# Performance work log

Hardware: AMD Instinct MI355X
Metric: run time of the kernel (lower is better)

The kernel has to match this reference:

```python
import jax, jax.numpy as jnp
import numpy as np

C_S, C_HID, H, P, V = 128, 16, 12, 4, 8
EPS = 1e-08
SOFTPLUS_INV_1 = 0.541324854612918


def _pts_from_linear(x, n_pts):
    # torch: split [..., 3*n] into 3 chunks of n, stack on dim=-1 -> [..., n, 3]
    B, N = x.shape[:2]
    return jnp.moveaxis(x.reshape(B, N, 3, n_pts), -2, -1)


def setup_inputs() -> dict:
    key = jax.random.key(0)
    ks = jax.random.split(key, 16)
    B, N = 2, 512
    hc = H * C_HID            # 192
    hpq = H * P * 3           # 144
    hpkv = H * (P + V) * 3    # 432
    cat_dim = H * (C_HID + V * 4)  # 576
    sc = 0.02
    inp = {
        "s": jax.random.normal(ks[0], (B, N, C_S), jnp.float32),
        "R": jax.random.normal(ks[1], (B, N, 3, 3), jnp.float32),
        "t": jax.random.normal(ks[2], (B, N, 3), jnp.float32),
        "pair_mask": jnp.ones((B, N, N), jnp.float32),
        "Wq": jax.random.normal(ks[3], (C_S, hc), jnp.float32) * sc,
        "bq": jnp.zeros((hc,), jnp.float32),
        "Wkv": jax.random.normal(ks[4], (C_S, 2 * hc), jnp.float32) * sc,
        "bkv": jnp.zeros((2 * hc,), jnp.float32),
        "Wqp": jax.random.normal(ks[5], (C_S, hpq), jnp.float32) * sc,
        "bqp": jnp.zeros((hpq,), jnp.float32),
        "Wkvp": jax.random.normal(ks[6], (C_S, hpkv), jnp.float32) * sc,
        "bkvp": jnp.zeros((hpkv,), jnp.float32),
        "head_weights": jnp.full((H,), SOFTPLUS_INV_1, jnp.float32),
        "Wout": jax.random.normal(ks[7], (cat_dim, C_S), jnp.float32) * sc,
        "bout": jnp.zeros((C_S,), jnp.float32),
    }
    return inp


def reference(s, R, t, pair_mask, Wq, bq, Wkv, bkv, Wqp, bqp, Wkvp, bkvp,
              head_weights, Wout, bout):
    B, N, _ = s.shape
    # scalar q/k/v
    q = (s @ Wq + bq).reshape(B, N, H, C_HID)
    kv = (s @ Wkv + bkv).reshape(B, N, H, 2 * C_HID)
    k, v = kv[..., :C_HID], kv[..., C_HID:]

    # point q/k/v in global frame: R x + t
    qp = _pts_from_linear(s @ Wqp + bqp, H * P)           # [B,N,HP,3]
    qp = jnp.einsum('bnij,bnpj->bnpi', R, qp) + t[:, :, None]
    qp = qp.reshape(B, N, H, P, 3)
    kvp = _pts_from_linear(s @ Wkvp + bkvp, H * (P + V))  # [B,N,H(P+V),3]
    kvp = jnp.einsum('bnij,bnpj->bnpi', R, kvp) + t[:, :, None]
    kvp = kvp.reshape(B, N, H, P + V, 3)
    kp, vp = kvp[..., :P, :], kvp[..., P:, :]

    # scalar attention logits [B,H,N,N]
    a = jnp.einsum('bihc,bjhc->bhij', q, k) * (1.0 / np.sqrt(3 * C_HID))

    # point-distance bias: sum_p ||q_i - k_j||^2 via |q|^2+|k|^2-2q.k
    sq_q = jnp.sum(qp * qp, axis=(-1, -2))   # [B,N,H]
    sq_k = jnp.sum(kp * kp, axis=(-1, -2))   # [B,N,H]
    cross = jnp.einsum('bihpc,bjhpc->bhij', qp, kp)
    d2 = (jnp.swapaxes(sq_q, 1, 2)[..., :, None]
          + jnp.swapaxes(sq_k, 1, 2)[..., None, :]
          - 2.0 * cross)                      # [B,H,N,N]
    hw = jax.nn.softplus(head_weights) * np.sqrt(1.0 / (3 * (P * 9.0 / 2)))
    pt_att = d2 * hw[None, :, None, None] * (-0.5)

    square_mask = 100000.0 * (pair_mask - 1.0)            # [B,N,N]
    a = jax.nn.softmax(a + pt_att + square_mask[:, None], axis=-1)

    # scalar output
    o = jnp.einsum('bhij,bjhc->bihc', a, v).reshape(B, N, H * C_HID)

    # point output, rotated back to local frame: R^T (x - t) form -> R^T x - t
    o_pt = jnp.einsum('bhij,bjhvc->bihvc', a, vp)         # [B,N,H,V,3]
    o_pt = jnp.einsum('bnji,bnhvj->bnhvi', R, o_pt) - t[:, :, None, None]
    o_pt_norm = jnp.sqrt(jnp.sum(o_pt * o_pt, axis=-1) + EPS).reshape(B, N, H * V)
    o_pt_flat = o_pt.reshape(B, N, H * V, 3)

    cat = jnp.concatenate(
        [o, o_pt_flat[..., 0], o_pt_flat[..., 1], o_pt_flat[..., 2], o_pt_norm],
        axis=-1)                                           # [B,N,576]
    return cat @ Wout + bout
```

## Files before the change

kernel.cpp:

```cpp
#include <hip/hip_runtime.h>
#include <hip/hip_bf16.h>
#include <math.h>

#define H_    12
#define B_    2
#define N_    512
#define BH_   (B_*H_)
#define QSCALE 0.14433756729740643f
#define CPT_K  0.13608276348795434f

#define OFF_QB   1356928
#define OFF_KP   1553536
#define OFF_VP   1750144
#define OFF_SA   2045056
#define OFF_SB   2057344
#define OFF_CATP 2069632

typedef __attribute__((ext_vector_type(8))) short sh8;
typedef __attribute__((ext_vector_type(4))) float f32x4;
typedef unsigned short u16t;

static __device__ __forceinline__ u16t f2b(float x) {
    __hip_bfloat16 h = __float2bfloat16(x);
    return *reinterpret_cast<u16t*>(&h);
}
static __device__ __forceinline__ int catp_idx(int tok, int col) {
    return (tok >> 4)*9216 + (col >> 5)*512 + ((col >> 3) & 3)*128
         + (tok & 15)*8 + (col & 7);
}

__global__ __launch_bounds__(512) void projpack_kernel(
    const float* __restrict__ s,
    const float* __restrict__ Rg, const float* __restrict__ tg,
    const float* __restrict__ hwg,
    const float* __restrict__ Wq,  const float* __restrict__ bq,
    const float* __restrict__ Wkv, const float* __restrict__ bkv,
    const float* __restrict__ Wqp, const float* __restrict__ bqp,
    const float* __restrict__ Wkvp,const float* __restrict__ bkvp,
    float* __restrict__ ws)
{
    __shared__ float ldsP[8][1160];

    u16t* Qb = (u16t*)(ws + OFF_QB);
    u16t* Kp = (u16t*)(ws + OFF_KP);
    u16t* Vp = (u16t*)(ws + OFF_VP);
    float* sa_g = ws + OFF_SA;
    float* sb_g = ws + OFF_SB;

    const int tid  = threadIdx.x;
    const int w    = tid >> 6, lane = tid & 63;
    const int kq   = lane >> 4, lx = lane & 15;
    const int half = blockIdx.x & 1;
    const int tok0 = (blockIdx.x >> 1) * 8;
    const int b    = tok0 >> 9, n0 = tok0 & 511;

    sh8 afr[4];
    #pragma unroll
    for (int ks = 0; ks < 4; ++ks) {
        const float* src = s + (tok0 + (lx & 7))*128 + ks*32 + kq*8;
        float4 u0 = *(const float4*)(src);
        float4 u1 = *(const float4*)(src+4);
        union { sh8 v; u16t u[8]; } pk;
        pk.u[0]=f2b(u0.x); pk.u[1]=f2b(u0.y); pk.u[2]=f2b(u0.z); pk.u[3]=f2b(u0.w);
        pk.u[4]=f2b(u1.x); pk.u[5]=f2b(u1.y); pk.u[6]=f2b(u1.z); pk.u[7]=f2b(u1.w);
        afr[ks] = pk.v;
    }

    const int gstart = (w < 4) ? w*5 : 20 + (w-4)*4;
    const int ng     = (w < 4) ? 5 : 4;

    for (int g = 0; g < ng; ++g) {
        int gg  = half*36 + gstart + g;
        int col = gg*16 + lx;
        const float* wsrc; int lc, od; float bv;
        if (col < 192)      { wsrc = Wq;   lc = col;     od = 192; bv = bq[lc]; }
        else if (col < 576) { wsrc = Wkv;  lc = col-192; od = 384; bv = bkv[lc]; }
        else if (col < 720) { wsrc = Wqp;  lc = col-576; od = 144; bv = bqp[lc]; }
        else                { wsrc = Wkvp; lc = col-720; od = 432; bv = bkvp[lc]; }

        f32x4 acc = {0.f,0.f,0.f,0.f};
        #pragma unroll
        for (int ks = 0; ks < 4; ++ks) {
            int k0 = ks*32 + kq*8;
            union { sh8 v; u16t u[8]; } pk;
            #pragma unroll
            for (int j = 0; j < 8; ++j) pk.u[j] = f2b(wsrc[(k0+j)*od + lc]);
            acc = __builtin_amdgcn_mfma_f32_16x16x32_bf16(afr[ks], pk.v, acc, 0, 0, 0);
        }
        if (kq < 2) {
            #pragma unroll
            for (int r = 0; r < 4; ++r)
                ldsP[kq*4 + r][gg*16 + lx] = acc[r] + bv;
        }
    }
    __syncthreads();

    if (half == 1) {
        for (int idx = tid; idx < 8*48; idx += 512) {
            int tk = idx / 48, p = idx % 48;
            int tok = tok0 + tk;
            const float* Rr = Rg + tok*9;
            const float* tr = tg + tok*3;
            float x0 = ldsP[tk][576 +  0 + p];
            float x1 = ldsP[tk][576 + 48 + p];
            float x2 = ldsP[tk][576 + 96 + p];
            ldsP[tk][576 +  0 + p] = Rr[0]*x0 + Rr[1]*x1 + Rr[2]*x2 + tr[0];
            ldsP[tk][576 + 48 + p] = Rr[3]*x0 + Rr[4]*x1 + Rr[5]*x2 + tr[1];
            ldsP[tk][576 + 96 + p] = Rr[6]*x0 + Rr[7]*x1 + Rr[8]*x2 + tr[2];
        }
        for (int idx = tid; idx < 8*144; idx += 512) {
            int tk = idx / 144, p = idx % 144;
            int tok = tok0 + tk;
            const float* Rr = Rg + tok*9;
            const float* tr = tg + tok*3;
            float x0 = ldsP[tk][720 +   0 + p];
            float x1 = ldsP[tk][720 + 144 + p];
            float x2 = ldsP[tk][720 + 288 + p];
            ldsP[tk][720 +   0 + p] = Rr[0]*x0 + Rr[1]*x1 + Rr[2]*x2 + tr[0];
            ldsP[tk][720 + 144 + p] = Rr[3]*x0 + Rr[4]*x1 + Rr[5]*x2 + tr[1];
            ldsP[tk][720 + 288 + p] = Rr[6]*x0 + Rr[7]*x1 + Rr[8]*x2 + tr[2];
        }
        __syncthreads();

        for (int idx = tid; idx < 8*12; idx += 512) {
            int tk = idx / 12, h = idx % 12;
            float hx = hwg[h];
            float sp = (hx > 20.f) ? hx : log1pf(__expf(hx));
            float qs = sp * CPT_K;
            union { sh8 v[2]; u16t u[16]; } pk;
            #pragma unroll
            for (int e = 0; e < 12; ++e)
                pk.u[e] = f2b(ldsP[tk][576 + (e%3)*48 + h*4 + e/3] * qs);
            pk.u[12]=0; pk.u[13]=0; pk.u[14]=0; pk.u[15]=0;
            u16t* dst = Qb + ((b*H_+h)*N_ + n0 + tk)*32 + 16;
            *(sh8*)dst = pk.v[0];
            *(sh8*)(dst+8) = pk.v[1];
        }
        for (int idx = tid; idx < 8*24; idx += 512) {
            int tk = idx / 24, r2 = idx % 24, h = r2 >> 1, fq = 2 + (r2 & 1);
            int j = n0 + tk, bh = b*H_ + h;
            union { sh8 v; u16t u[8]; } pk;
            #pragma unroll
            for (int e = 0; e < 8; ++e) {
                int c = fq*8 + e;
                float val;
                if (c < 28) val = ldsP[tk][720 + ((c-16)%3)*144 + h*12 + (c-16)/3];
                else        val = 0.f;
                pk.u[e] = f2b(val);
            }
            *(sh8*)(Kp + bh*16384 + (j>>4)*512 + fq*128 + (j&15)*8) = pk.v;
        }
        for (int idx = tid; idx < 12*24; idx += 512) {
            int h = idx / 24, d = 16 + idx % 24;
            int bh = b*H_ + h;
            union { sh8 v; u16t u[8]; } pk;
            #pragma unroll
            for (int e = 0; e < 8; ++e)
                pk.u[e] = f2b(ldsP[e][720 + ((d-16)%3)*144 + h*12 + 4 + (d-16)/3]);
            int j = n0;
            *(sh8*)(Vp + bh*24576 + (j>>5)*1536 + (d>>4)*512 + ((j>>3)&3)*128
                    + (d&15)*8) = pk.v;
        }
        for (int idx = tid; idx < 8*12; idx += 512) {
            int tk = idx / 12, h = idx % 12;
            float hx = hwg[h];
            float sp = (hx > 20.f) ? hx : log1pf(__expf(hx));
            float c_pt = -0.5f * sp * CPT_K;
            float sq = 0.f, sk = 0.f;
            #pragma unroll
            for (int pp = 0; pp < 4; ++pp)
                #pragma unroll
                for (int c = 0; c < 3; ++c) {
                    float a = ldsP[tk][576 + c*48  + h*4  + pp]; sq += a*a;
                    float k = ldsP[tk][720 + c*144 + h*12 + pp]; sk += k*k;
                }
            sa_g[(b*H_+h)*N_ + n0 + tk] = c_pt * sq;
            sb_g[(b*H_+h)*N_ + n0 + tk] = c_pt * sk;
        }
    } else {
        for (int idx = tid; idx < 8*12; idx += 512) {
            int tk = idx / 12, h = idx % 12;
            union { sh8 v[2]; u16t u[16]; } pk;
            #pragma unroll
            for (int e = 0; e < 16; ++e) pk.u[e] = f2b(ldsP[tk][h*16 + e] * QSCALE);
            u16t* dst = Qb + ((b*H_+h)*N_ + n0 + tk)*32;
            *(sh8*)dst = pk.v[0];
            *(sh8*)(dst+8) = pk.v[1];
        }
        for (int idx = tid; idx < 8*24; idx += 512) {
            int tk = idx / 24, r2 = idx % 24, h = r2 >> 1, fq = r2 & 1;
            int j = n0 + tk, bh = b*H_ + h;
            union { sh8 v; u16t u[8]; } pk;
            #pragma unroll
            for (int e = 0; e < 8; ++e)
                pk.u[e] = f2b(ldsP[tk][192 + h*32 + fq*8 + e]);
            *(sh8*)(Kp + bh*16384 + (j>>4)*512 + fq*128 + (j&15)*8) = pk.v;
        }
        for (int idx = tid; idx < 12*16; idx += 512) {
            int h = idx / 16, d = idx % 16;
            int bh = b*H_ + h;
            union { sh8 v; u16t u[8]; } pk;
            #pragma unroll
            for (int e = 0; e < 8; ++e)
                pk.u[e] = f2b(ldsP[e][192 + h*32 + 16 + d]);
            int j = n0;
            *(sh8*)(Vp + bh*24576 + (j>>5)*1536 + (d>>4)*512 + ((j>>3)&3)*128
                    + (d&15)*8) = pk.v;
        }
    }
}

__global__ __launch_bounds__(256, 3) void attn_kernel(
    const float* __restrict__ Rg, const float* __restrict__ tg,
    const float* __restrict__ maskg, float* __restrict__ ws)
{
    __shared__ u16t smP[4*16*72];
    __shared__ float mbuf[3*64*20];
    __shared__ float obuf[16*32];

    const u16t* Qb = (const u16t*)(ws + OFF_QB);
    const u16t* Kp = (const u16t*)(ws + OFF_KP);
    const u16t* Vp = (const u16t*)(ws + OFF_VP);
    const float* sa_g = ws + OFF_SA;
    const float* sb_g = ws + OFF_SB;
    u16t* catp = (u16t*)(ws + OFF_CATP);

    const int tid  = threadIdx.x;
    const int jh   = tid >> 6, lane = tid & 63;
    const int kq   = lane >> 4, lx = lane & 15;
    const int bh   = blockIdx.x >> 5;
    const int it   = blockIdx.x & 31;
    const int b    = bh / H_, h = bh % H_;
    const int i0   = it * 16;

    sh8 qfrag = *(const sh8*)(Qb + (bh*N_ + i0 + lx)*32 + kq*8);
    float sa_r[4];
    #pragma unroll
    for (int r = 0; r < 4; ++r)
        sa_r[r] = sa_g[bh*N_ + i0 + kq*4 + r];

    float m_run[4] = {-1e30f,-1e30f,-1e30f,-1e30f};
    float l_run[4] = {0.f,0.f,0.f,0.f};
    f32x4 oc0 = {0.f,0.f,0.f,0.f}, oc1 = oc0, oc2 = oc0;

    const float* mrow = maskg + (size_t)(b*N_ + i0 + kq*4)*N_ + lx;
    u16t* pw = smP + jh*1152;

    #pragma unroll
    for (int t = 0; t < 2; ++t) {
        const int jt = jh*2 + t;
        const int j0 = jt * 64;

        f32x4 sc[4];
        #pragma unroll
        for (int st = 0; st < 4; ++st) {
            sh8 kf = *(const sh8*)(Kp + bh*16384 + (jt*4+st)*512 + kq*128 + lx*8);
            f32x4 z = {0.f,0.f,0.f,0.f};
            sc[st] = __builtin_amdgcn_mfma_f32_16x16x32_bf16(qfrag, kf, z, 0, 0, 0);
        }
        float sbv[4];
        #pragma unroll
        for (int st = 0; st < 4; ++st) sbv[st] = sb_g[bh*N_ + j0 + st*16 + lx];
        float mb[16];
        #pragma unroll
        for (int r = 0; r < 4; ++r)
            #pragma unroll
            for (int st = 0; st < 4; ++st)
                mb[r*4+st] = mrow[r*N_ + j0 + st*16];

        float L[16];
        #pragma unroll
        for (int st = 0; st < 4; ++st)
            #pragma unroll
            for (int r = 0; r < 4; ++r)
                L[st*4+r] = sc[st][r] + sa_r[r] + sbv[st] + 1e5f*(mb[r*4+st] - 1.f);

        #pragma unroll
        for (int r = 0; r < 4; ++r) {
            float tm = fmaxf(fmaxf(L[0*4+r], L[1*4+r]), fmaxf(L[2*4+r], L[3*4+r]));
            tm = fmaxf(tm, __shfl_xor(tm, 1));
            tm = fmaxf(tm, __shfl_xor(tm, 2));
            tm = fmaxf(tm, __shfl_xor(tm, 4));
            tm = fmaxf(tm, __shfl_xor(tm, 8));
            float mnew = fmaxf(m_run[r], tm);
            float al = __expf(m_run[r] - mnew);
            m_run[r] = mnew;
            l_run[r] *= al;
            oc0[r] *= al; oc1[r] *= al; oc2[r] *= al;
        }
        #pragma unroll
        for (int st = 0; st < 4; ++st)
            #pragma unroll
            for (int r = 0; r < 4; ++r) {
                float p = __expf(L[st*4+r] - m_run[r]);
                l_run[r] += p;
                pw[(kq*4+r)*72 + st*16 + lx] = f2b(p);
            }
        #pragma unroll
        for (int c = 0; c < 2; ++c) {
            sh8 pa = *(const sh8*)(pw + lx*72 + c*32 + kq*8);
            #pragma unroll
            for (int nq = 0; nq < 3; ++nq) {
                sh8 vf = *(const sh8*)(Vp + bh*24576 + (jt*2+c)*1536 + nq*512
                                        + kq*128 + lx*8);
                if (nq == 0) oc0 = __builtin_amdgcn_mfma_f32_16x16x32_bf16(pa, vf, oc0, 0,0,0);
                if (nq == 1) oc1 = __builtin_amdgcn_mfma_f32_16x16x32_bf16(pa, vf, oc1, 0,0,0);
                if (nq == 2) oc2 = __builtin_amdgcn_mfma_f32_16x16x32_bf16(pa, vf, oc2, 0,0,0);
            }
        }
    }

    if (jh > 0) {
        float* mb = mbuf + ((jh-1)*64 + lane)*20;
        #pragma unroll
        for (int r = 0; r < 4; ++r) {
            mb[r]      = m_run[r];
            mb[4 + r]  = l_run[r];
            mb[8 + r]  = oc0[r];
            mb[12 + r] = oc1[r];
            mb[16 + r] = oc2[r];
        }
    }
    __syncthreads();
    if (jh == 0) {
        float linv[4];
        #pragma unroll
        for (int r = 0; r < 4; ++r) {
            float ms = m_run[r];
            #pragma unroll
            for (int q = 0; q < 3; ++q)
                ms = fmaxf(ms, mbuf[(q*64 + lane)*20 + r]);
            float eA = __expf(m_run[r] - ms);
            float l = l_run[r]*eA;
            oc0[r] *= eA; oc1[r] *= eA; oc2[r] *= eA;
            #pragma unroll
            for (int q = 0; q < 3; ++q) {
                const float* mb = mbuf + (q*64 + lane)*20;
                float e = __expf(mb[r] - ms);
                l      += mb[4+r]*e;
                oc0[r] += mb[8+r]*e;
                oc1[r] += mb[12+r]*e;
                oc2[r] += mb[16+r]*e;
            }
            l += __shfl_xor(l, 1); l += __shfl_xor(l, 2);
            l += __shfl_xor(l, 4); l += __shfl_xor(l, 8);
            linv[r] = 1.f / l;
        }

        #pragma unroll
        for (int r = 0; r < 4; ++r) {
            int row = kq*4 + r;
            int tok = b*N_ + i0 + row;
            catp[catp_idx(tok, h*16 + lx)] = f2b(oc0[r] * linv[r]);
            obuf[row*32 + lx]      = oc1[r] * linv[r];
            obuf[row*32 + 16 + lx] = oc2[r] * linv[r];
        }

        #pragma unroll
        for (int tsk = 0; tsk < 2; ++tsk) {
            int task = lane + tsk*64;
            int r = task >> 3, pv = task & 7;
            int tok = b*N_ + i0 + r;
            const float* Rr = Rg + tok*9;
            const float* tr = tg + tok*3;
            float g0 = obuf[r*32 + pv*3 + 0];
            float g1 = obuf[r*32 + pv*3 + 1];
            float g2 = obuf[r*32 + pv*3 + 2];
            float px = Rr[0]*g0 + Rr[3]*g1 + Rr[6]*g2 - tr[0];
            float py = Rr[1]*g0 + Rr[4]*g1 + Rr[7]*g2 - tr[1];
            float pz = Rr[2]*g0 + Rr[5]*g1 + Rr[8]*g2 - tr[2];
            float nrm = sqrtf(px*px + py*py + pz*pz + 1e-8f);
            catp[catp_idx(tok, 192 + h*8 + pv)] = f2b(px);
            catp[catp_idx(tok, 288 + h*8 + pv)] = f2b(py);
            catp[catp_idx(tok, 384 + h*8 + pv)] = f2b(pz);
            catp[catp_idx(tok, 480 + h*8 + pv)] = f2b(nrm);
        }
    }
}

__global__ __launch_bounds__(512) void out_kernel(
    const float* __restrict__ Wout, const float* __restrict__ bout,
    const float* __restrict__ ws, float* __restrict__ out)
{
    __shared__ float part[2][3][64][4];

    const int tid = threadIdx.x;
    const int w = tid >> 6, lane = tid & 63;
    const int cg = w & 1, kh = w >> 1;
    const int lx = lane & 15, kq = lane >> 4;
    const int nt = blockIdx.x, mt = blockIdx.y;

    const sh8* Ap = (const sh8*)((const u16t*)(ws + OFF_CATP));

    const int col = nt*32 + cg*16 + lx;
    const int ke0 = (kh*18) >> 2;
    const int ke1 = ((kh+1)*18) >> 2;

    f32x4 acc = {0.f,0.f,0.f,0.f};
    #pragma unroll 5
    for (int ks = ke0; ks < ke1; ++ks) {
        sh8 af = Ap[((mt*18 + ks)*4 + kq)*16 + lx];
        int k0 = ks*32 + kq*8;
        union { sh8 v; u16t u[8]; } pk;
        #pragma unroll
        for (int j = 0; j < 8; ++j) pk.u[j] = f2b(Wout[(k0+j)*128 + col]);
        acc = __builtin_amdgcn_mfma_f32_16x16x32_bf16(af, pk.v, acc, 0, 0, 0);
    }
    if (kh > 0) {
        #pragma unroll
        for (int r = 0; r < 4; ++r) part[cg][kh-1][lane][r] = acc[r];
    }
    __syncthreads();
    if (kh == 0) {
        float bv = bout[col];
        #pragma unroll
        for (int r = 0; r < 4; ++r) {
            int row = mt*16 + kq*4 + r;
            out[row*128 + col] = acc[r] + part[cg][0][lane][r]
                               + part[cg][1][lane][r] + part[cg][2][lane][r] + bv;
        }
    }
}

extern "C" void kernel_launch(void* const* d_in, const int* in_sizes, int n_in,
                              void* d_out, int out_size, void* d_ws, size_t ws_size,
                              hipStream_t stream) {
    const float* s    = (const float*)d_in[0];
    const float* R    = (const float*)d_in[1];
    const float* t    = (const float*)d_in[2];
    const float* mask = (const float*)d_in[3];
    const float* Wq   = (const float*)d_in[4];
    const float* bq   = (const float*)d_in[5];
    const float* Wkv  = (const float*)d_in[6];
    const float* bkv  = (const float*)d_in[7];
    const float* Wqp  = (const float*)d_in[8];
    const float* bqp  = (const float*)d_in[9];
    const float* Wkvp = (const float*)d_in[10];
    const float* bkvp = (const float*)d_in[11];
    const float* hw   = (const float*)d_in[12];
    const float* Wout = (const float*)d_in[13];
    const float* bout = (const float*)d_in[14];
    float* ws  = (float*)d_ws;
    float* out = (float*)d_out;

    projpack_kernel<<<256, 512, 0, stream>>>(s, R, t, hw, Wq, bq, Wkv, bkv,
                                             Wqp, bqp, Wkvp, bkvp, ws);
    attn_kernel<<<BH_*32, 256, 0, stream>>>(R, t, mask, ws);
    out_kernel<<<dim3(4, 64), 512, 0, stream>>>(Wout, bout, ws, out);
}
```

Measured before the change: 106.2 us.

## Parallelize attention epilogue merge across waves and split out GEMM K finer

The attention kernel's final softmax-merge is now done by two waves instead of one: every wave dumps its partial state to shared memory, wave 0 produces the scalar output and wave 1 the point outputs, then 128 threads do the frame rotation and norms. The output GEMM kernel switches from 2 column groups × 4 K-splits to 1 column group × 8 K-splits per block, doubling the grid to 8×64 blocks. Both aim to shorten serial tails and raise parallelism, at the cost of an extra barrier, more shared memory and more partial-sum reduction work.

```diff
diff --git a/kernel.cpp b/kernel.cpp
--- a/kernel.cpp
+++ b/kernel.cpp
@@ -215,7 +215,7 @@
     const float* __restrict__ maskg, float* __restrict__ ws)
 {
     __shared__ u16t smP[4*16*72];
-    __shared__ float mbuf[3*64*20];
+    __shared__ float mbuf[4*64*20];
     __shared__ float obuf[16*32];
 
     const u16t* Qb = (const u16t*)(ws + OFF_QB);
@@ -310,8 +310,8 @@
         }
     }
 
-    if (jh > 0) {
-        float* mb = mbuf + ((jh-1)*64 + lane)*20;
+    {
+        float* mb = mbuf + (jh*64 + lane)*20;
         #pragma unroll
         for (int r = 0; r < 4; ++r) {
             mb[r]      = m_run[r];
@@ -322,59 +322,65 @@
         }
     }
     __syncthreads();
-    if (jh == 0) {
+
+    if (jh < 2) {
         float linv[4];
+        f32x4 mo0, mo1, mo2;
         #pragma unroll
         for (int r = 0; r < 4; ++r) {
-            float ms = m_run[r];
-            #pragma unroll
-            for (int q = 0; q < 3; ++q)
+            float ms = -1e30f;
+            #pragma unroll
+            for (int q = 0; q < 4; ++q)
                 ms = fmaxf(ms, mbuf[(q*64 + lane)*20 + r]);
-            float eA = __expf(m_run[r] - ms);
-            float l = l_run[r]*eA;
-            oc0[r] *= eA; oc1[r] *= eA; oc2[r] *= eA;
-            #pragma unroll
-            for (int q = 0; q < 3; ++q) {
+            float l = 0.f, o0 = 0.f, o1 = 0.f, o2 = 0.f;
+            #pragma unroll
+            for (int q = 0; q < 4; ++q) {
                 const float* mb = mbuf + (q*64 + lane)*20;
                 float e = __expf(mb[r] - ms);
-                l      += mb[4+r]*e;
-                oc0[r] += mb[8+r]*e;
-                oc1[r] += mb[12+r]*e;
-                oc2[r] += mb[16+r]*e;
+                l  += mb[4 + r]*e;
+                o0 += mb[8 + r]*e;
+                o1 += mb[12 + r]*e;
+                o2 += mb[16 + r]*e;
             }
             l += __shfl_xor(l, 1); l += __shfl_xor(l, 2);
             l += __shfl_xor(l, 4); l += __shfl_xor(l, 8);
             linv[r] = 1.f / l;
-        }
-
-        #pragma unroll
-        for (int r = 0; r < 4; ++r) {
-            int row = kq*4 + r;
-            int tok = b*N_ + i0 + row;
-            catp[catp_idx(tok, h*16 + lx)] = f2b(oc0[r] * linv[r]);
-            obuf[row*32 + lx]      = oc1[r] * linv[r];
-            obuf[row*32 + 16 + lx] = oc2[r] * linv[r];
-        }
-
-        #pragma unroll
-        for (int tsk = 0; tsk < 2; ++tsk) {
-            int task = lane + tsk*64;
-            int r = task >> 3, pv = task & 7;
-            int tok = b*N_ + i0 + r;
-            const float* Rr = Rg + tok*9;
-            const float* tr = tg + tok*3;
-            float g0 = obuf[r*32 + pv*3 + 0];
-            float g1 = obuf[r*32 + pv*3 + 1];
-            float g2 = obuf[r*32 + pv*3 + 2];
-            float px = Rr[0]*g0 + Rr[3]*g1 + Rr[6]*g2 - tr[0];
-            float py = Rr[1]*g0 + Rr[4]*g1 + Rr[7]*g2 - tr[1];
-            float pz = Rr[2]*g0 + Rr[5]*g1 + Rr[8]*g2 - tr[2];
-            float nrm = sqrtf(px*px + py*py + pz*pz + 1e-8f);
-            catp[catp_idx(tok, 192 + h*8 + pv)] = f2b(px);
-            catp[catp_idx(tok, 288 + h*8 + pv)] = f2b(py);
-            catp[catp_idx(tok, 384 + h*8 + pv)] = f2b(pz);
-            catp[catp_idx(tok, 480 + h*8 + pv)] = f2b(nrm);
-        }
+            mo0[r] = o0; mo1[r] = o1; mo2[r] = o2;
+        }
+
+        if (jh == 0) {
+            #pragma unroll
+            for (int r = 0; r < 4; ++r) {
+                int tok = b*N_ + i0 + kq*4 + r;
+                catp[catp_idx(tok, h*16 + lx)] = f2b(mo0[r] * linv[r]);
+            }
+        } else {
+            #pragma unroll
+            for (int r = 0; r < 4; ++r) {
+                int row = kq*4 + r;
+                obuf[row*32 + lx]      = mo1[r] * linv[r];
+                obuf[row*32 + 16 + lx] = mo2[r] * linv[r];
+            }
+        }
+    }
+    __syncthreads();
+
+    if (tid < 128) {
+        int r = tid >> 3, pv = tid & 7;
+        int tok = b*N_ + i0 + r;
+        const float* Rr = Rg + tok*9;
+        const float* tr = tg + tok*3;
+        float g0 = obuf[r*32 + pv*3 + 0];
+        float g1 = obuf[r*32 + pv*3 + 1];
+        float g2 = obuf[r*32 + pv*3 + 2];
+        float px = Rr[0]*g0 + Rr[3]*g1 + Rr[6]*g2 - tr[0];
+        float py = Rr[1]*g0 + Rr[4]*g1 + Rr[7]*g2 - tr[1];
+        float pz = Rr[2]*g0 + Rr[5]*g1 + Rr[8]*g2 - tr[2];
+        float nrm = sqrtf(px*px + py*py + pz*pz + 1e-8f);
+        catp[catp_idx(tok, 192 + h*8 + pv)] = f2b(px);
+        catp[catp_idx(tok, 288 + h*8 + pv)] = f2b(py);
+        catp[catp_idx(tok, 384 + h*8 + pv)] = f2b(pz);
+        catp[catp_idx(tok, 480 + h*8 + pv)] = f2b(nrm);
     }
 }
 
@@ -382,22 +388,21 @@
     const float* __restrict__ Wout, const float* __restrict__ bout,
     const float* __restrict__ ws, float* __restrict__ out)
 {
-    __shared__ float part[2][3][64][4];
+    __shared__ float part[7][64][4];
 
     const int tid = threadIdx.x;
-    const int w = tid >> 6, lane = tid & 63;
-    const int cg = w & 1, kh = w >> 1;
+    const int kh = tid >> 6, lane = tid & 63;
     const int lx = lane & 15, kq = lane >> 4;
     const int nt = blockIdx.x, mt = blockIdx.y;
 
     const sh8* Ap = (const sh8*)((const u16t*)(ws + OFF_CATP));
 
-    const int col = nt*32 + cg*16 + lx;
-    const int ke0 = (kh*18) >> 2;
-    const int ke1 = ((kh+1)*18) >> 2;
+    const int col = nt*16 + lx;
+    const int ke0 = (kh*18) >> 3;
+    const int ke1 = ((kh+1)*18) >> 3;
 
     f32x4 acc = {0.f,0.f,0.f,0.f};
-    #pragma unroll 5
+    #pragma unroll 3
     for (int ks = ke0; ks < ke1; ++ks) {
         sh8 af = Ap[((mt*18 + ks)*4 + kq)*16 + lx];
         int k0 = ks*32 + kq*8;
@@ -408,16 +413,18 @@
     }
     if (kh > 0) {
         #pragma unroll
-        for (int r = 0; r < 4; ++r) part[cg][kh-1][lane][r] = acc[r];
+        for (int r = 0; r < 4; ++r) part[kh-1][lane][r] = acc[r];
     }
     __syncthreads();
     if (kh == 0) {
         float bv = bout[col];
         #pragma unroll
         for (int r = 0; r < 4; ++r) {
+            float v = acc[r];
+            #pragma unroll
+            for (int p = 0; p < 7; ++p) v += part[p][lane][r];
             int row = mt*16 + kq*4 + r;
-            out[row*128 + col] = acc[r] + part[cg][0][lane][r]
-                               + part[cg][1][lane][r] + part[cg][2][lane][r] + bv;
+            out[row*128 + col] = v + bv;
         }
     }
 }
@@ -446,5 +453,5 @@
     projpack_kernel<<<256, 512, 0, stream>>>(s, R, t, hw, Wq, bq, Wkv, bkv,
                                              Wqp, bqp, Wkvp, bkvp, ws);
     attn_kernel<<<BH_*32, 256, 0, stream>>>(R, t, mask, ws);
-    out_kernel<<<dim3(4, 64), 512, 0, stream>>>(Wout, bout, ws, out);
-}
+    out_kernel<<<dim3(8, 64), 512, 0, stream>>>(Wout, bout, ws, out);
+}
```

After: 108.3 us. Within noise of the previous version (+1.9%).
